# Kernel optimization log

Measured on AMD Instinct MI355X. Metric: run time of the kernel, lower is better.

Reference implementation:

```python
import jax, jax.numpy as jnp
import numpy as np

B, TQ, TV, D = 8, 2048, 2048, 128
NEG = 1e9  # keras Attention uses additive -1e9 masking for fp32


def setup_inputs() -> dict:
    key = jax.random.key(0)
    kq, kv, kk, kmq, kmv = jax.random.split(key, 5)
    q = jax.random.normal(kq, (B, TQ, D), dtype=jnp.float32)
    v = jax.random.normal(kv, (B, TV, D), dtype=jnp.float32)
    k = jax.random.normal(kk, (B, TV, D), dtype=jnp.float32)
    # learned scalar scale from use_scale=True, initialized to ones
    scale = jnp.ones((), dtype=jnp.float32)
    mask_q = jax.random.randint(kmq, (B, TQ), 0, 2) > 0
    mask_v = jax.random.randint(kmv, (B, TV), 0, 2) > 0
    return {"q": q, "v": v, "k": k, "scale": scale, "mask_q": mask_q, "mask_v": mask_v}


def reference(q, v, k, scale, mask_q, mask_v):
    # scores: [B, Tq, Tv]
    scores = scale * jnp.einsum('bqd,bkd->bqk', q, k)
    # key/value mask: additive -1e9 on masked positions (keras semantics)
    scores = scores - NEG * (1.0 - mask_v[:, None, :].astype(scores.dtype))
    weights = jax.nn.softmax(scores, axis=-1)
    out = jnp.einsum('bqk,bkd->bqd', weights, v)
    # query mask zeroes out masked query rows
    out = out * mask_q[:, :, None].astype(out.dtype)
    return out
```

## Files before the change

kernel.cpp:

```cpp
#include <hip/hip_runtime.h>
#include <cstddef>

#define NB 8
#define TQ 2048
#define TV 2048
#define DD 128
#define KVT 32
#define NWV 4
#define CHW (TV / NWV)
#define NT  (CHW / KVT)
#define LOG2E 1.4426950408889634f

typedef _Float16 f16x8 __attribute__((ext_vector_type(8)));
typedef _Float16 f16x4 __attribute__((ext_vector_type(4)));
typedef float f32x4 __attribute__((ext_vector_type(4)));

__device__ __forceinline__ float fast_exp2(float x) {
  return __builtin_amdgcn_exp2f(x);
}

__global__ __launch_bounds__(256) void prepass_kernel(
    const float* __restrict__ k, const float* __restrict__ v,
    const int* __restrict__ mask_v,
    _Float16* __restrict__ kh2, _Float16* __restrict__ vt2,
    _Float16* __restrict__ indb)
{
  __shared__ _Float16 tlds[32 * 34];
  const int tid = threadIdx.x;
  const int bid = blockIdx.x;
  if (bid < 512) {
    int b = bid >> 6, kt = bid & 63;
    int row = tid >> 3, d0 = (tid & 7) * 4;
    int R = 16 * ((row >> 2) & 1) + 4 * (row >> 3) + (row & 3);
    const float* src = k + ((size_t)(b * TV + kt * 32 + row)) * DD;
    _Float16* dst = kh2 + ((size_t)(b * 64 + kt)) * 4096;
#pragma unroll
    for (int it = 0; it < 4; ++it) {
      float4 x = *(const float4*)(src + it * 32 + d0);
      f16x4 h; h[0] = (_Float16)x.x; h[1] = (_Float16)x.y;
      h[2] = (_Float16)x.z; h[3] = (_Float16)x.w;
      *(f16x4*)(dst + it * 1024 + R * 32 + d0) = h;
    }
  } else if (bid < 512 + 2048) {
    int tb = bid - 512;
    int b = tb >> 8, rem = tb & 255;
    int kt = rem >> 2, dt = rem & 3;
    int r = tid >> 3, c0 = (tid & 7) * 4;
    float mfac = (mask_v[(size_t)b * TV + kt * 32 + r] != 0) ? 1.f : 0.f;
    float4 x = *(const float4*)&v[((size_t)b * TV + kt * 32 + r) * DD + dt * 32 + c0];
    tlds[(c0 + 0) * 34 + r] = (_Float16)(mfac * x.x);
    tlds[(c0 + 1) * 34 + r] = (_Float16)(mfac * x.y);
    tlds[(c0 + 2) * 34 + r] = (_Float16)(mfac * x.z);
    tlds[(c0 + 3) * 34 + r] = (_Float16)(mfac * x.w);
    __syncthreads();
    int dl = tid >> 3, k0 = (tid & 7) * 4;
    f16x4 h;
#pragma unroll
    for (int i = 0; i < 4; ++i) h[i] = tlds[dl * 34 + k0 + i];
    size_t eidx = (((size_t)b * 64 + kt) * 128 + (dt * 32 + dl)) * 32 + k0;
    *(f16x4*)&vt2[eidx] = h;
  } else {
    int bid2 = bid - 512 - 2048;
    size_t base = (size_t)bid2 * 1024 + tid * 4;
#pragma unroll
    for (int i = 0; i < 4; ++i)
      indb[base + i] = (mask_v[base + i] != 0) ? (_Float16)1.f : (_Float16)0.f;
  }
}

__global__ __launch_bounds__(256, 2) void attn_main(
    const float* __restrict__ q, const float* __restrict__ scale_p,
    const _Float16* __restrict__ kh2, const _Float16* __restrict__ vt2,
    const _Float16* __restrict__ indb,
    const int* __restrict__ mask_q, float* __restrict__ out)
{
  __shared__ __align__(16) float osh[32 * 132];
  __shared__ float msh[NWV][32], lsh[NWV][32];

  const int tid = threadIdx.x;
  const int w = tid >> 6;
  const int lane = tid & 63;
  const int l15 = lane & 15, lg = lane >> 4;

  const int b = blockIdx.x & 7;
  const int qg = blockIdx.x >> 3;
  const int qbase = qg * 32;

  const _Float16* ktiles = kh2 + (size_t)b * 64 * 4096;
  const _Float16* vtiles = vt2 + (size_t)b * 64 * 4096;
  const _Float16* indbt = indb + (size_t)b * TV;

  const float sc2 = scale_p[0] * LOG2E;
  f16x8 qf[2][4];
#pragma unroll
  for (int rb = 0; rb < 2; ++rb)
#pragma unroll
    for (int kc = 0; kc < 4; ++kc) {
      const float* qp = q + ((size_t)b * TQ + qbase + rb * 16 + l15) * DD + kc * 32 + lg * 8;
      float4 xa = *(const float4*)qp;
      float4 xb = *(const float4*)(qp + 4);
      f16x8 h;
      h[0] = (_Float16)(sc2 * xa.x); h[1] = (_Float16)(sc2 * xa.y);
      h[2] = (_Float16)(sc2 * xa.z); h[3] = (_Float16)(sc2 * xa.w);
      h[4] = (_Float16)(sc2 * xb.x); h[5] = (_Float16)(sc2 * xb.y);
      h[6] = (_Float16)(sc2 * xb.z); h[7] = (_Float16)(sc2 * xb.w);
      qf[rb][kc] = h;
    }

  f32x4 acc[2][8];
  f32x4 accl[2];
#pragma unroll
  for (int rb = 0; rb < 2; ++rb) {
    accl[rb] = (f32x4){0.f, 0.f, 0.f, 0.f};
#pragma unroll
    for (int ct = 0; ct < 8; ++ct) acc[rb][ct] = (f32x4){0.f, 0.f, 0.f, 0.f};
  }
  float m[2];
  m[0] = -3.0e38f; m[1] = -3.0e38f;

  const int tbase = w * NT;

  f16x8 kbuf[2][8];
  f16x8 indbuf[2];

  {
    const _Float16* kt0 = ktiles + (size_t)tbase * 4096;
#pragma unroll
    for (int kc = 0; kc < 4; ++kc) {
      kbuf[0][2 * kc]     = *(const f16x8*)(kt0 + kc * 1024 + l15 * 32 + lg * 8);
      kbuf[0][2 * kc + 1] = *(const f16x8*)(kt0 + kc * 1024 + (16 + l15) * 32 + lg * 8);
    }
    indbuf[0] = *(const f16x8*)(indbt + tbase * 32 + lg * 8);
  }

#pragma unroll
  for (int t = 0; t < NT; ++t) {
    const int p = t & 1;
    const int tile = tbase + t;

    f32x4 s[2][2];
    s[0][0] = (f32x4){0,0,0,0}; s[0][1] = (f32x4){0,0,0,0};
    s[1][0] = (f32x4){0,0,0,0}; s[1][1] = (f32x4){0,0,0,0};
    __builtin_amdgcn_s_setprio(1);
#pragma unroll
    for (int kc = 0; kc < 4; ++kc) {
      s[0][0] = __builtin_amdgcn_mfma_f32_16x16x32_f16(kbuf[p][2*kc],   qf[0][kc], s[0][0], 0, 0, 0);
      s[0][1] = __builtin_amdgcn_mfma_f32_16x16x32_f16(kbuf[p][2*kc],   qf[1][kc], s[0][1], 0, 0, 0);
      s[1][0] = __builtin_amdgcn_mfma_f32_16x16x32_f16(kbuf[p][2*kc+1], qf[0][kc], s[1][0], 0, 0, 0);
      s[1][1] = __builtin_amdgcn_mfma_f32_16x16x32_f16(kbuf[p][2*kc+1], qf[1][kc], s[1][1], 0, 0, 0);
    }
    __builtin_amdgcn_s_setprio(0);

    const _Float16* vtb = vtiles + (size_t)tile * 4096;
    f16x8 vf[8];
#pragma unroll
    for (int ct = 0; ct < 8; ++ct)
      vf[ct] = *(const f16x8*)(vtb + (ct * 16 + l15) * 32 + lg * 8);

    if (t + 1 < NT) {
      const _Float16* ktn = ktiles + (size_t)(tile + 1) * 4096;
#pragma unroll
      for (int kc = 0; kc < 4; ++kc) {
        kbuf[p ^ 1][2 * kc]     = *(const f16x8*)(ktn + kc * 1024 + l15 * 32 + lg * 8);
        kbuf[p ^ 1][2 * kc + 1] = *(const f16x8*)(ktn + kc * 1024 + (16 + l15) * 32 + lg * 8);
      }
      indbuf[p ^ 1] = *(const f16x8*)(indbt + (tile + 1) * 32 + lg * 8);
    }

    const f16x8 indf = indbuf[p];

    f16x8 pa[2];
#pragma unroll
    for (int rb = 0; rb < 2; ++rb) {
#pragma unroll
      for (int r = 0; r < 4; ++r) {
        s[0][rb][r] += ((float)indf[r]     - 1.f) * 60000.f;
        s[1][rb][r] += ((float)indf[4 + r] - 1.f) * 60000.f;
      }
      float lm = fmaxf(fmaxf(fmaxf(s[0][rb][0], s[0][rb][1]), fmaxf(s[0][rb][2], s[0][rb][3])),
                       fmaxf(fmaxf(s[1][rb][0], s[1][rb][1]), fmaxf(s[1][rb][2], s[1][rb][3])));
      if (__any(lm > m[rb] + 11.5f)) {
        float pm = lm;
        pm = fmaxf(pm, __shfl_xor(pm, 16, 64));
        pm = fmaxf(pm, __shfl_xor(pm, 32, 64));
        float mn = fmaxf(m[rb], pm);
        float alpha = fast_exp2(m[rb] - mn);
        m[rb] = mn;
        f32x4 alv;
#pragma unroll
        for (int r = 0; r < 4; ++r)
          alv[r] = __shfl(alpha, lg * 4 + r, 64);
        accl[rb] *= alv;
#pragma unroll
        for (int ct = 0; ct < 8; ++ct) acc[rb][ct] *= alv;
      }
      f16x8 pp;
      pp[0] = (_Float16)fast_exp2(s[0][rb][0] - m[rb]);
      pp[1] = (_Float16)fast_exp2(s[0][rb][1] - m[rb]);
      pp[2] = (_Float16)fast_exp2(s[0][rb][2] - m[rb]);
      pp[3] = (_Float16)fast_exp2(s[0][rb][3] - m[rb]);
      pp[4] = (_Float16)fast_exp2(s[1][rb][0] - m[rb]);
      pp[5] = (_Float16)fast_exp2(s[1][rb][1] - m[rb]);
      pp[6] = (_Float16)fast_exp2(s[1][rb][2] - m[rb]);
      pp[7] = (_Float16)fast_exp2(s[1][rb][3] - m[rb]);
      pa[rb] = pp;
    }

    __builtin_amdgcn_s_setprio(1);
#pragma unroll
    for (int ct = 0; ct < 8; ++ct) {
      acc[0][ct] = __builtin_amdgcn_mfma_f32_16x16x32_f16(pa[0], vf[ct], acc[0][ct], 0, 0, 0);
      acc[1][ct] = __builtin_amdgcn_mfma_f32_16x16x32_f16(pa[1], vf[ct], acc[1][ct], 0, 0, 0);
    }
    accl[0] = __builtin_amdgcn_mfma_f32_16x16x32_f16(pa[0], indf, accl[0], 0, 0, 0);
    accl[1] = __builtin_amdgcn_mfma_f32_16x16x32_f16(pa[1], indf, accl[1], 0, 0, 0);
    __builtin_amdgcn_s_setprio(0);
  }

  if (lg == 0) {
    msh[w][l15]      = m[0];
    msh[w][16 + l15] = m[1];
  }
  if (l15 == 0) {
#pragma unroll
    for (int rb = 0; rb < 2; ++rb)
#pragma unroll
      for (int r = 0; r < 4; ++r)
        lsh[w][rb * 16 + lg * 4 + r] = accl[rb][r];
  }
  __syncthreads();

  float coef[2][4];
#pragma unroll
  for (int rb = 0; rb < 2; ++rb)
#pragma unroll
    for (int r = 0; r < 4; ++r) {
      int row = rb * 16 + lg * 4 + r;
      float mstar = msh[0][row];
#pragma unroll
      for (int wv = 1; wv < NWV; ++wv) mstar = fmaxf(mstar, msh[wv][row]);
      coef[rb][r] = fast_exp2(msh[w][row] - mstar);
    }

#pragma unroll
  for (int wv = 0; wv < NWV; ++wv) {
    if (w == wv) {
#pragma unroll
      for (int rb = 0; rb < 2; ++rb)
#pragma unroll
        for (int ct = 0; ct < 8; ++ct)
#pragma unroll
          for (int r = 0; r < 4; ++r) {
            int idx = (rb * 16 + lg * 4 + r) * 132 + ct * 16 + l15;
            float val = coef[rb][r] * acc[rb][ct][r];
            if (wv == 0) osh[idx] = val; else osh[idx] += val;
          }
    }
    __syncthreads();
  }

  {
    const int row = tid >> 3;
    const int cg = (tid & 7) * 16;
    float mstar = msh[0][row];
#pragma unroll
    for (int wv = 1; wv < NWV; ++wv) mstar = fmaxf(mstar, msh[wv][row]);
    float lstar = 0.f;
#pragma unroll
    for (int wv = 0; wv < NWV; ++wv)
      lstar += fast_exp2(msh[wv][row] - mstar) * lsh[wv][row];
    const int qr = qbase + row;
    const float f = ((mask_q[(size_t)b * TQ + qr] != 0) ? 1.f : 0.f) / lstar;
    float* orow = out + ((size_t)b * TQ + qr) * DD + cg;
#pragma unroll
    for (int i4 = 0; i4 < 4; ++i4) {
      float4 p = *(float4*)&osh[row * 132 + cg + i4 * 4];
      float4 o; o.x = p.x * f; o.y = p.y * f; o.z = p.z * f; o.w = p.w * f;
      *(float4*)(orow + i4 * 4) = o;
    }
  }
}

__global__ __launch_bounds__(64, 4) void attn_f32_kernel(
    const float* __restrict__ q, const float* __restrict__ v,
    const float* __restrict__ k, const float* __restrict__ scale_p,
    const int* __restrict__ mask_q, const int* __restrict__ mask_v,
    float* __restrict__ out)
{
  __shared__ __align__(16) _Float16 plds[16 * 40];
  const int lane = threadIdx.x & 63;
  const int l15 = lane & 15, lg = lane >> 4;
  const int qblocks = TQ / 16;
  const int b = blockIdx.x / qblocks, qb = blockIdx.x % qblocks;
  const int qbase = qb * 16;
  const float scale = scale_p[0];
  const float* qp = q + ((size_t)b * TQ + qbase) * DD;
  const float* kbase = k + (size_t)b * TV * DD;
  const float* vbase = v + (size_t)b * TV * DD;
  const int* mvb = mask_v + b * TV;
  f16x8 qf[4];
#pragma unroll
  for (int kc = 0; kc < 4; ++kc) {
    float4 a = *(const float4*)(qp + (size_t)l15 * DD + kc * 32 + lg * 8);
    float4 bb = *(const float4*)(qp + (size_t)l15 * DD + kc * 32 + lg * 8 + 4);
    f16x8 h; h[0]=(_Float16)a.x;h[1]=(_Float16)a.y;h[2]=(_Float16)a.z;h[3]=(_Float16)a.w;
    h[4]=(_Float16)bb.x;h[5]=(_Float16)bb.y;h[6]=(_Float16)bb.z;h[7]=(_Float16)bb.w;
    qf[kc]=h;
  }
  f32x4 acc[8];
#pragma unroll
  for (int i = 0; i < 8; ++i) acc[i] = (f32x4){0.f,0.f,0.f,0.f};
  float m[4], lsum[4];
#pragma unroll
  for (int r = 0; r < 4; ++r) { m[r] = -3.0e38f; lsum[r] = 0.f; }
  for (int kt = 0; kt < TV; kt += KVT) {
    f32x4 s0 = {0,0,0,0}, s1 = {0,0,0,0};
#pragma unroll
    for (int kc = 0; kc < 4; ++kc) {
      const float* kp0 = kbase + (size_t)(kt + l15) * DD + kc * 32 + lg * 8;
      float4 a = *(const float4*)kp0; float4 bb = *(const float4*)(kp0 + 4);
      f16x8 kf0; kf0[0]=(_Float16)a.x;kf0[1]=(_Float16)a.y;kf0[2]=(_Float16)a.z;kf0[3]=(_Float16)a.w;
      kf0[4]=(_Float16)bb.x;kf0[5]=(_Float16)bb.y;kf0[6]=(_Float16)bb.z;kf0[7]=(_Float16)bb.w;
      s0 = __builtin_amdgcn_mfma_f32_16x16x32_f16(qf[kc], kf0, s0, 0, 0, 0);
      const float* kp1 = kbase + (size_t)(kt + 16 + l15) * DD + kc * 32 + lg * 8;
      a = *(const float4*)kp1; bb = *(const float4*)(kp1 + 4);
      f16x8 kf1; kf1[0]=(_Float16)a.x;kf1[1]=(_Float16)a.y;kf1[2]=(_Float16)a.z;kf1[3]=(_Float16)a.w;
      kf1[4]=(_Float16)bb.x;kf1[5]=(_Float16)bb.y;kf1[6]=(_Float16)bb.z;kf1[7]=(_Float16)bb.w;
      s1 = __builtin_amdgcn_mfma_f32_16x16x32_f16(qf[kc], kf1, s1, 0, 0, 0);
    }
    const float a0 = (mvb[kt + l15] != 0) ? 0.f : -1e9f;
    const float a1 = (mvb[kt + 16 + l15] != 0) ? 0.f : -1e9f;
    float pmx[4];
#pragma unroll
    for (int r = 0; r < 4; ++r) {
      s0[r] = s0[r] * scale + a0; s1[r] = s1[r] * scale + a1;
      pmx[r] = fmaxf(s0[r], s1[r]);
    }
#pragma unroll
    for (int off = 1; off < 16; off <<= 1)
#pragma unroll
      for (int r = 0; r < 4; ++r) pmx[r] = fmaxf(pmx[r], __shfl_xor(pmx[r], off, 64));
    float al[4], ps[4];
#pragma unroll
    for (int r = 0; r < 4; ++r) {
      float mn = fmaxf(m[r], pmx[r]);
      al[r] = __expf(m[r] - mn); m[r] = mn;
      float p0 = __expf(s0[r] - mn), p1 = __expf(s1[r] - mn);
      ps[r] = p0 + p1;
      int row = lg * 4 + r;
      plds[row * 40 + l15] = (_Float16)p0;
      plds[row * 40 + 16 + l15] = (_Float16)p1;
    }
#pragma unroll
    for (int off = 1; off < 16; off <<= 1)
#pragma unroll
      for (int r = 0; r < 4; ++r) ps[r] += __shfl_xor(ps[r], off, 64);
#pragma unroll
    for (int r = 0; r < 4; ++r) {
      lsum[r] = lsum[r] * al[r] + ps[r];
#pragma unroll
      for (int ct = 0; ct < 8; ++ct) acc[ct][r] *= al[r];
    }
    f16x8 pa = *(const f16x8*)&plds[l15 * 40 + lg * 8];
#pragma unroll
    for (int ct = 0; ct < 8; ++ct) {
      const float* vp = vbase + (size_t)(kt + lg * 8) * DD + ct * 16 + l15;
      f16x8 vfx;
#pragma unroll
      for (int j = 0; j < 8; ++j) vfx[j] = (_Float16)vp[(size_t)j * DD];
      acc[ct] = __builtin_amdgcn_mfma_f32_16x16x32_f16(pa, vfx, acc[ct], 0, 0, 0);
    }
  }
  const int* mqb = mask_q + b * TQ;
#pragma unroll
  for (int r = 0; r < 4; ++r) {
    int row = lg * 4 + r;
    int qr = qbase + row;
    float f = ((mqb[qr] != 0) ? 1.f : 0.f) / lsum[r];
    float* orow = out + ((size_t)b * TQ + qr) * DD;
#pragma unroll
    for (int ct = 0; ct < 8; ++ct) orow[ct * 16 + l15] = acc[ct][r] * f;
  }
}

extern "C" void kernel_launch(void* const* d_in, const int* in_sizes, int n_in,
                              void* d_out, int out_size, void* d_ws, size_t ws_size,
                              hipStream_t stream) {
  const float* q      = (const float*)d_in[0];
  const float* v      = (const float*)d_in[1];
  const float* k      = (const float*)d_in[2];
  const float* scale  = (const float*)d_in[3];
  const int*   mask_q = (const int*)d_in[4];
  const int*   mask_v = (const int*)d_in[5];
  float* out = (float*)d_out;

  const size_t kvBytes = 2ull * NB * TV * DD * sizeof(_Float16);
  const size_t indBytes = (size_t)NB * TV * sizeof(_Float16);
  if (ws_size >= kvBytes + indBytes) {
    _Float16* kh2 = (_Float16*)d_ws;
    _Float16* vt2 = kh2 + (size_t)NB * TV * DD;
    _Float16* indb = vt2 + (size_t)NB * TV * DD;
    hipLaunchKernelGGL(prepass_kernel, dim3(512 + 2048 + 16), dim3(256), 0, stream,
                       k, v, mask_v, kh2, vt2, indb);
    hipLaunchKernelGGL(attn_main, dim3(NB * (TQ / 32)), dim3(256), 0, stream,
                       q, scale, kh2, vt2, indb, mask_q, out);
  } else {
    hipLaunchKernelGGL(attn_f32_kernel, dim3(NB * (TQ / 16)), dim3(64), 0, stream,
                       q, v, k, scale, mask_q, mask_v, out);
  }
}
```

Measured before the change: 53.07 us.

## Software-pipeline QK of next tile with softmax/PV of current tile

Restructures the KV tile loop into a two-stage software pipeline with ping-pong score buffers (sA/sB). The QK^T MFMAs for tile t+1 are issued before the softmax and PV MFMAs of tile t, and the K, V and indicator loads are interleaved to overlap with compute. The aim is to hide exp/softmax VALU latency and memory latency behind matrix work. In exchange it keeps a second score buffer live, which raises register pressure. It also relies on NT being even.

```diff
diff --git a/kernel.cpp b/kernel.cpp
--- a/kernel.cpp
+++ b/kernel.cpp
@@ -120,55 +120,37 @@
 
   const int tbase = w * NT;
 
-  f16x8 kbuf[2][8];
-  f16x8 indbuf[2];
-
-  {
-    const _Float16* kt0 = ktiles + (size_t)tbase * 4096;
+  f16x8 kbuf[8], vbuf[8];
+  f16x8 ib0, ib1;
+
+  auto load_k = [&](int tile) {
+    const _Float16* ktb = ktiles + (size_t)tile * 4096;
 #pragma unroll
     for (int kc = 0; kc < 4; ++kc) {
-      kbuf[0][2 * kc]     = *(const f16x8*)(kt0 + kc * 1024 + l15 * 32 + lg * 8);
-      kbuf[0][2 * kc + 1] = *(const f16x8*)(kt0 + kc * 1024 + (16 + l15) * 32 + lg * 8);
-    }
-    indbuf[0] = *(const f16x8*)(indbt + tbase * 32 + lg * 8);
-  }
-
-#pragma unroll
-  for (int t = 0; t < NT; ++t) {
-    const int p = t & 1;
-    const int tile = tbase + t;
-
-    f32x4 s[2][2];
+      kbuf[2 * kc]     = *(const f16x8*)(ktb + kc * 1024 + l15 * 32 + lg * 8);
+      kbuf[2 * kc + 1] = *(const f16x8*)(ktb + kc * 1024 + (16 + l15) * 32 + lg * 8);
+    }
+  };
+  auto load_v = [&](int tile) {
+    const _Float16* vtb = vtiles + (size_t)tile * 4096;
+#pragma unroll
+    for (int ct = 0; ct < 8; ++ct)
+      vbuf[ct] = *(const f16x8*)(vtb + (ct * 16 + l15) * 32 + lg * 8);
+  };
+  auto do_qk = [&](f32x4 (&s)[2][2]) {
     s[0][0] = (f32x4){0,0,0,0}; s[0][1] = (f32x4){0,0,0,0};
     s[1][0] = (f32x4){0,0,0,0}; s[1][1] = (f32x4){0,0,0,0};
     __builtin_amdgcn_s_setprio(1);
 #pragma unroll
     for (int kc = 0; kc < 4; ++kc) {
-      s[0][0] = __builtin_amdgcn_mfma_f32_16x16x32_f16(kbuf[p][2*kc],   qf[0][kc], s[0][0], 0, 0, 0);
-      s[0][1] = __builtin_amdgcn_mfma_f32_16x16x32_f16(kbuf[p][2*kc],   qf[1][kc], s[0][1], 0, 0, 0);
-      s[1][0] = __builtin_amdgcn_mfma_f32_16x16x32_f16(kbuf[p][2*kc+1], qf[0][kc], s[1][0], 0, 0, 0);
-      s[1][1] = __builtin_amdgcn_mfma_f32_16x16x32_f16(kbuf[p][2*kc+1], qf[1][kc], s[1][1], 0, 0, 0);
+      s[0][0] = __builtin_amdgcn_mfma_f32_16x16x32_f16(kbuf[2*kc],   qf[0][kc], s[0][0], 0, 0, 0);
+      s[0][1] = __builtin_amdgcn_mfma_f32_16x16x32_f16(kbuf[2*kc],   qf[1][kc], s[0][1], 0, 0, 0);
+      s[1][0] = __builtin_amdgcn_mfma_f32_16x16x32_f16(kbuf[2*kc+1], qf[0][kc], s[1][0], 0, 0, 0);
+      s[1][1] = __builtin_amdgcn_mfma_f32_16x16x32_f16(kbuf[2*kc+1], qf[1][kc], s[1][1], 0, 0, 0);
     }
     __builtin_amdgcn_s_setprio(0);
-
-    const _Float16* vtb = vtiles + (size_t)tile * 4096;
-    f16x8 vf[8];
-#pragma unroll
-    for (int ct = 0; ct < 8; ++ct)
-      vf[ct] = *(const f16x8*)(vtb + (ct * 16 + l15) * 32 + lg * 8);
-
-    if (t + 1 < NT) {
-      const _Float16* ktn = ktiles + (size_t)(tile + 1) * 4096;
-#pragma unroll
-      for (int kc = 0; kc < 4; ++kc) {
-        kbuf[p ^ 1][2 * kc]     = *(const f16x8*)(ktn + kc * 1024 + l15 * 32 + lg * 8);
-        kbuf[p ^ 1][2 * kc + 1] = *(const f16x8*)(ktn + kc * 1024 + (16 + l15) * 32 + lg * 8);
-      }
-      indbuf[p ^ 1] = *(const f16x8*)(indbt + (tile + 1) * 32 + lg * 8);
-    }
-
-    const f16x8 indf = indbuf[p];
-
+  };
+  auto do_sm_pv = [&](f32x4 (&s)[2][2], const f16x8& indf) {
     f16x8 pa[2];
 #pragma unroll
     for (int rb = 0; rb < 2; ++rb) {
@@ -205,16 +187,43 @@
       pp[7] = (_Float16)fast_exp2(s[1][rb][3] - m[rb]);
       pa[rb] = pp;
     }
-
     __builtin_amdgcn_s_setprio(1);
 #pragma unroll
     for (int ct = 0; ct < 8; ++ct) {
-      acc[0][ct] = __builtin_amdgcn_mfma_f32_16x16x32_f16(pa[0], vf[ct], acc[0][ct], 0, 0, 0);
-      acc[1][ct] = __builtin_amdgcn_mfma_f32_16x16x32_f16(pa[1], vf[ct], acc[1][ct], 0, 0, 0);
+      acc[0][ct] = __builtin_amdgcn_mfma_f32_16x16x32_f16(pa[0], vbuf[ct], acc[0][ct], 0, 0, 0);
+      acc[1][ct] = __builtin_amdgcn_mfma_f32_16x16x32_f16(pa[1], vbuf[ct], acc[1][ct], 0, 0, 0);
     }
     accl[0] = __builtin_amdgcn_mfma_f32_16x16x32_f16(pa[0], indf, accl[0], 0, 0, 0);
     accl[1] = __builtin_amdgcn_mfma_f32_16x16x32_f16(pa[1], indf, accl[1], 0, 0, 0);
     __builtin_amdgcn_s_setprio(0);
+  };
+
+  f32x4 sA[2][2], sB[2][2];
+
+  load_k(tbase);
+  ib0 = *(const f16x8*)(indbt + tbase * 32 + lg * 8);
+  do_qk(sA);
+  load_k(tbase + 1);
+  ib1 = *(const f16x8*)(indbt + (tbase + 1) * 32 + lg * 8);
+  load_v(tbase);
+
+#pragma unroll
+  for (int tp = 0; tp < NT / 2; ++tp) {
+    const int t0 = 2 * tp;
+    do_qk(sB);
+    if (t0 + 2 < NT) load_k(tbase + t0 + 2);
+    do_sm_pv(sA, ib0);
+    load_v(tbase + t0 + 1);
+    if (t0 + 2 < NT) ib0 = *(const f16x8*)(indbt + (tbase + t0 + 2) * 32 + lg * 8);
+    if (t0 + 2 < NT) {
+      do_qk(sA);
+      if (t0 + 3 < NT) load_k(tbase + t0 + 3);
+    }
+    do_sm_pv(sB, ib1);
+    if (t0 + 2 < NT) {
+      load_v(tbase + t0 + 2);
+      if (t0 + 3 < NT) ib1 = *(const f16x8*)(indbt + (tbase + t0 + 3) * 32 + lg * 8);
+    }
   }
 
   if (lg == 0) {
```

Measured after the change: 53.30 us. About the same (+0.4%).
